# Performance work log

Hardware: AMD Instinct MI355X
Metric: run time of the kernel (lower is better)

Reference implementation:

```python
import jax, jax.numpy as jnp
import numpy as np

N_NODES = 50000
N_EDGES = 400000
IN_CH = 109
OUT_CH = 32


def setup_inputs() -> dict:
    key = jax.random.key(0)
    ks = jax.random.split(key, 12)
    dims = [(IN_CH, 10 * OUT_CH), (10 * OUT_CH, 2 * OUT_CH), (2 * OUT_CH, OUT_CH), (2 * OUT_CH, OUT_CH)]
    inp = {
        'x': jax.random.normal(ks[0], (N_NODES, IN_CH), dtype=jnp.float32),
        'edge_index': jax.random.randint(ks[1], (2, N_EDGES), 0, N_NODES, dtype=jnp.int64) if jax.config.jax_enable_x64 else jax.random.randint(ks[1], (2, N_EDGES), 0, N_NODES, dtype=jnp.int32),
    }
    names = ['W1', 'b1', 'W2', 'b2', 'Wmu', 'bmu', 'Wls', 'bls']
    for i, (fi, fo) in enumerate(dims):
        scale = 1.0 / np.sqrt(fi)
        inp[names[2 * i]] = jax.random.uniform(ks[2 + 2 * i], (fi, fo), minval=-scale, maxval=scale, dtype=jnp.float32)
        inp[names[2 * i + 1]] = jnp.zeros((fo,), dtype=jnp.float32)
    return inp


def _gcn_conv(x, src, dst, norm, W, b, n):
    # PyG GCNConv: h = x @ W, then symmetric-normalized aggregation, then + b
    h = x @ W                                   # [N, F_out]
    msg = h[src] * norm[:, None]                # [E+N, F_out]
    out = jax.ops.segment_sum(msg, dst, num_segments=n)
    return out + b


def _norm_and_loops(edge_index, n):
    # add self loops, compute D^{-1/2}(A+I)D^{-1/2} edge weights
    loops = jnp.arange(n, dtype=edge_index.dtype)
    src = jnp.concatenate([edge_index[0], loops])
    dst = jnp.concatenate([edge_index[1], loops])
    deg = jax.ops.segment_sum(jnp.ones_like(src, dtype=jnp.float32), dst, num_segments=n)
    dinv = jnp.where(deg > 0, jax.lax.rsqrt(jnp.maximum(deg, 1.0)), 0.0)
    norm = dinv[src] * dinv[dst]
    return src, dst, norm


def reference(x, edge_index, W1, b1, W2, b2, Wmu, bmu, Wls, bls):
    n = x.shape[0]
    src, dst, norm = _norm_and_loops(edge_index, n)
    h = jax.nn.relu(_gcn_conv(x, src, dst, norm, W1, b1, n))
    h = jax.nn.relu(_gcn_conv(h, src, dst, norm, W2, b2, n))
    mu = _gcn_conv(h, src, dst, norm, Wmu, bmu, n)
    logstd = _gcn_conv(h, src, dst, norm, Wls, bls, n)
    return (mu, logstd)
```

## Files before the change

### kernel.cpp

```cpp
#include <hip/hip_runtime.h>

#define NN 50000
#define NE 400000

typedef __attribute__((ext_vector_type(8))) short short8v;
typedef __attribute__((ext_vector_type(4))) float f32x4;

__device__ __forceinline__ unsigned short f2bf_rtn(float x) {
    unsigned u = __float_as_uint(x);
    unsigned r = u + 0x7FFFu + ((u >> 16) & 1u);
    return (unsigned short)(r >> 16);
}
__device__ __forceinline__ float bf2f(unsigned short h) {
    return __uint_as_float(((unsigned)h) << 16);
}

__global__ void prep_kernel(const float* __restrict__ x,
                            const float* __restrict__ W1, const float* __restrict__ W2,
                            const float* __restrict__ Wmu, const float* __restrict__ Wls,
                            unsigned* __restrict__ xp, int* __restrict__ zero_base,
                            unsigned short* __restrict__ w1t_hi,
                            unsigned short* __restrict__ w2t_hi,
                            unsigned short* __restrict__ wct_hi) {
    int b = blockIdx.x, tid = threadIdx.x;
    if (b < 12500) {
        int idx = b * 256 + tid;
        int i = idx >> 6, c2 = (idx & 63) * 2;
        long xb = (long)i * 109;
        float v0 = (c2 < 109) ? x[xb + c2] : 0.0f;
        float v1 = (c2 + 1 < 109) ? x[xb + c2 + 1] : 0.0f;
        xp[idx] = (unsigned)f2bf_rtn(v0) | ((unsigned)f2bf_rtn(v1) << 16);
    } else if (b < 12891) {
        int i = (b - 12500) * 256 + tid;
        if (i < 100096) zero_base[i] = 0;
    } else if (b < 13051) {
        int idx = (b - 12891) * 256 + tid;
        int n = idx >> 7, k = idx & 127;
        float v = (k < 109) ? W1[(long)k * 320 + n] : 0.0f;
        w1t_hi[idx] = f2bf_rtn(v);
    } else if (b < 13131) {
        int idx = (b - 13051) * 256 + tid;
        int n = idx / 320, k = idx - n * 320;
        w2t_hi[idx] = f2bf_rtn(W2[(long)k * 64 + n]);
    } else {
        int idx = (b - 13131) * 256 + tid;
        int n = idx >> 6, k = idx & 63;
        float v = (n < 32) ? Wmu[k * 32 + n] : Wls[k * 32 + (n - 32)];
        wct_hi[idx] = f2bf_rtn(v);
    }
}

__global__ void hist_kernel(const int* __restrict__ dst, int* __restrict__ counts) {
    for (int e = blockIdx.x * blockDim.x + threadIdx.x; e < NE; e += gridDim.x * blockDim.x)
        atomicAdd(&counts[dst[e]], 1);
}

__global__ void dinv_scan1_kernel(const int* __restrict__ counts, float* __restrict__ dinv,
                                  int* __restrict__ rowstart, int* __restrict__ bsum) {
    __shared__ int tmp[256];
    int tid = threadIdx.x;
    int i = blockIdx.x * 256 + tid;
    int v = (i < NN) ? counts[i] : 0;
    if (i < NN) dinv[i] = rsqrtf((float)(v + 1));
    tmp[tid] = v;
    __syncthreads();
    for (int off = 1; off < 256; off <<= 1) {
        int t = 0;
        if (tid >= off) t = tmp[tid - off];
        __syncthreads();
        if (tid >= off) tmp[tid] += t;
        __syncthreads();
    }
    if (i < NN) rowstart[i] = tmp[tid] - v;
    if (tid == 255) bsum[blockIdx.x] = tmp[255];
}

__global__ void scan23_kernel(int* __restrict__ rowstart, const int* __restrict__ bsum) {
    __shared__ int red[4];
    int tid = threadIdx.x;
    int v = (tid < 196 && tid < (int)blockIdx.x) ? bsum[tid] : 0;
    for (int off = 32; off > 0; off >>= 1) v += __shfl_down(v, off, 64);
    if ((tid & 63) == 0) red[tid >> 6] = v;
    __syncthreads();
    int pref = red[0] + red[1] + red[2] + red[3];
    int i = blockIdx.x * 256 + tid;
    if (i < NN) rowstart[i] += pref;
    if (i == 0) rowstart[NN] = NE;
}

__global__ void scatter_kernel(const int* __restrict__ src, const int* __restrict__ dst,
                               const int* __restrict__ rowstart, int* __restrict__ cursor,
                               int* __restrict__ esrc) {
    for (int e = blockIdx.x * blockDim.x + threadIdx.x; e < NE; e += gridDim.x * blockDim.x) {
        int d = dst[e];
        int pos = rowstart[d] + atomicAdd(&cursor[d], 1);
        esrc[pos] = src[e];
    }
}

__global__ __launch_bounds__(256) void agg109_packed_kernel(const int* __restrict__ rowstart,
                                                            const int* __restrict__ esrc,
                                                            const float* __restrict__ dinv,
                                                            const unsigned* __restrict__ xp,
                                                            unsigned* __restrict__ xa_hi32) {
    int wave = blockIdx.x * (blockDim.x >> 6) + (threadIdx.x >> 6);
    if (wave >= NN) return;
    int lane = threadIdx.x & 63;
    float wd = dinv[wave];
    unsigned pself = xp[(long)wave * 64 + lane];
    float acc0 = __uint_as_float(pself << 16) * wd;
    float acc1 = __uint_as_float(pself & 0xFFFF0000u) * wd;
    int j0 = rowstart[wave], j1 = rowstart[wave + 1];
    int j = j0;
    for (; j + 8 <= j1; j += 8) {
        int s[8];
        float w[8];
        unsigned pp[8];
        #pragma unroll
        for (int u = 0; u < 8; ++u) s[u] = esrc[j + u];
        #pragma unroll
        for (int u = 0; u < 8; ++u) w[u] = dinv[s[u]];
        #pragma unroll
        for (int u = 0; u < 8; ++u) pp[u] = xp[(long)s[u] * 64 + lane];
        #pragma unroll
        for (int u = 0; u < 8; ++u) {
            acc0 = fmaf(__uint_as_float(pp[u] << 16), w[u], acc0);
            acc1 = fmaf(__uint_as_float(pp[u] & 0xFFFF0000u), w[u], acc1);
        }
    }
    for (; j + 4 <= j1; j += 4) {
        int s0 = esrc[j], s1 = esrc[j + 1], s2 = esrc[j + 2], s3 = esrc[j + 3];
        float w0 = dinv[s0], w1 = dinv[s1], w2 = dinv[s2], w3 = dinv[s3];
        unsigned p0 = xp[(long)s0 * 64 + lane], p1 = xp[(long)s1 * 64 + lane];
        unsigned p2 = xp[(long)s2 * 64 + lane], p3 = xp[(long)s3 * 64 + lane];
        acc0 = fmaf(__uint_as_float(p0 << 16), w0, acc0);
        acc1 = fmaf(__uint_as_float(p0 & 0xFFFF0000u), w0, acc1);
        acc0 = fmaf(__uint_as_float(p1 << 16), w1, acc0);
        acc1 = fmaf(__uint_as_float(p1 & 0xFFFF0000u), w1, acc1);
        acc0 = fmaf(__uint_as_float(p2 << 16), w2, acc0);
        acc1 = fmaf(__uint_as_float(p2 & 0xFFFF0000u), w2, acc1);
        acc0 = fmaf(__uint_as_float(p3 << 16), w3, acc0);
        acc1 = fmaf(__uint_as_float(p3 & 0xFFFF0000u), w3, acc1);
    }
    for (; j < j1; ++j) {
        int s = esrc[j];
        float w = dinv[s];
        unsigned pv = xp[(long)s * 64 + lane];
        acc0 = fmaf(__uint_as_float(pv << 16), w, acc0);
        acc1 = fmaf(__uint_as_float(pv & 0xFFFF0000u), w, acc1);
    }
    acc0 *= wd;
    acc1 *= wd;
    xa_hi32[(long)wave * 64 + lane] =
        (unsigned)f2bf_rtn(acc0) | ((unsigned)f2bf_rtn(acc1) << 16);
}

#define LDA_T 136
#define LDH 328

__global__ __launch_bounds__(256) void gemm12_kernel(const unsigned short* __restrict__ xa,
                                                     const unsigned short* __restrict__ w1t,
                                                     const unsigned short* __restrict__ w2t,
                                                     const float* __restrict__ b1,
                                                     const float* __restrict__ dinv,
                                                     unsigned short* __restrict__ g2b) {
    __shared__ unsigned short As[64 * LDA_T];
    __shared__ unsigned short Bs[64 * LDA_T];
    __shared__ unsigned short Hs[64 * LDH];
    int tid = threadIdx.x;
    int wid = tid >> 6, lane = tid & 63;
    int l15 = lane & 15, l4 = lane >> 4;

    int T = gridDim.x;
    int xcd = blockIdx.x & 7, jj = blockIdx.x >> 3;
    int q = T >> 3, r = T & 7;
    int start = (xcd < r) ? xcd * (q + 1) : r * (q + 1) + (xcd - r) * q;
    int bm0 = (start + jj) * 64;

    #pragma unroll
    for (int r2 = 0; r2 < 4; ++r2) {
        int idx = tid + 256 * r2;
        int row = idx >> 4, slot = idx & 15;
        int grow = bm0 + row;
        if (grow >= NN) grow = NN - 1;
        *(uint4*)&As[row * LDA_T + slot * 8] = *(const uint4*)&xa[(long)grow * 128 + slot * 8];
    }
    #pragma unroll
    for (int r2 = 0; r2 < 4; ++r2) {
        int idx = tid + 256 * r2;
        int row = idx >> 4, slot = idx & 15;
        *(uint4*)&Bs[row * LDA_T + slot * 8] = *(const uint4*)&w1t[(long)row * 128 + slot * 8];
    }
    __syncthreads();

    for (int nc = 0; nc < 5; ++nc) {
        f32x4 acc[4] = {};
        #pragma unroll
        for (int ks = 0; ks < 4; ++ks) {
            int koff = ks * 32 + l4 * 8;
            short8v ah = *(const short8v*)&As[(wid * 16 + l15) * LDA_T + koff];
            #pragma unroll
            for (int n = 0; n < 4; ++n) {
                short8v bh = *(const short8v*)&Bs[(n * 16 + l15) * LDA_T + koff];
                acc[n] = __builtin_amdgcn_mfma_f32_16x16x32_bf16(ah, bh, acc[n], 0, 0, 0);
            }
        }
        int rbase = wid * 16 + l4 * 4;
        #pragma unroll
        for (int q2 = 0; q2 < 4; ++q2) {
            #pragma unroll
            for (int n = 0; n < 4; ++n) {
                int gcol = nc * 64 + n * 16 + l15;
                float v = acc[n][q2] + b1[gcol];
                v = v > 0.0f ? v : 0.0f;
                Hs[(rbase + q2) * LDH + gcol] = f2bf_rtn(v);
            }
        }
        __syncthreads();
        if (nc < 4) {
            #pragma unroll
            for (int r2 = 0; r2 < 4; ++r2) {
                int idx = tid + 256 * r2;
                int row = idx >> 4, slot = idx & 15;
                *(uint4*)&Bs[row * LDA_T + slot * 8] =
                    *(const uint4*)&w1t[(long)(nc * 64 + 64 + row) * 128 + slot * 8];
            }
            __syncthreads();
        }
    }

    f32x4 acc2[4] = {};
    for (int kc = 0; kc < 5; ++kc) {
        #pragma unroll
        for (int r2 = 0; r2 < 2; ++r2) {
            int idx = tid + 256 * r2;
            int row = idx >> 3, slot = idx & 7;
            *(uint4*)&Bs[row * LDA_T + slot * 8] =
                *(const uint4*)&w2t[(long)row * 320 + kc * 64 + slot * 8];
        }
        __syncthreads();
        #pragma unroll
        for (int ks = 0; ks < 2; ++ks) {
            int koff = ks * 32 + l4 * 8;
            short8v ah = *(const short8v*)&Hs[(wid * 16 + l15) * LDH + kc * 64 + koff];
            #pragma unroll
            for (int n = 0; n < 4; ++n) {
                short8v bh = *(const short8v*)&Bs[(n * 16 + l15) * LDA_T + koff];
                acc2[n] = __builtin_amdgcn_mfma_f32_16x16x32_bf16(ah, bh, acc2[n], 0, 0, 0);
            }
        }
        __syncthreads();
    }
    int rbase = bm0 + wid * 16 + l4 * 4;
    #pragma unroll
    for (int q2 = 0; q2 < 4; ++q2) {
        int grow = rbase + q2;
        if (grow >= NN) continue;
        float rs = dinv[grow];
        #pragma unroll
        for (int n = 0; n < 4; ++n) {
            int gcol = n * 16 + l15;
            g2b[(long)grow * 64 + gcol] = f2bf_rtn(acc2[n][q2] * rs);
        }
    }
}

__global__ __launch_bounds__(256) void agg64_relu_bf16_kernel(const int* __restrict__ rowstart,
                                                              const int* __restrict__ esrc,
                                                              const float* __restrict__ dinv,
                                                              const unsigned short* __restrict__ g,
                                                              const float* __restrict__ b,
                                                              unsigned short* __restrict__ hhi) {
    int wave = blockIdx.x * (blockDim.x >> 6) + (threadIdx.x >> 6);
    if (wave >= NN) return;
    int lane = threadIdx.x & 63;
    long base = (long)wave * 64;
    float acc = bf2f(g[base + lane]);
    int j0 = rowstart[wave], j1 = rowstart[wave + 1];
    int j = j0;
    for (; j + 8 <= j1; j += 8) {
        int s[8];
        float pp[8];
        #pragma unroll
        for (int u = 0; u < 8; ++u) s[u] = esrc[j + u];
        #pragma unroll
        for (int u = 0; u < 8; ++u) pp[u] = bf2f(g[(long)s[u] * 64 + lane]);
        #pragma unroll
        for (int u = 0; u < 8; ++u) acc += pp[u];
    }
    for (; j + 4 <= j1; j += 4) {
        int s0 = esrc[j], s1 = esrc[j + 1], s2 = esrc[j + 2], s3 = esrc[j + 3];
        float p0 = bf2f(g[(long)s0 * 64 + lane]), p1 = bf2f(g[(long)s1 * 64 + lane]);
        float p2 = bf2f(g[(long)s2 * 64 + lane]), p3 = bf2f(g[(long)s3 * 64 + lane]);
        acc += p0 + p1 + p2 + p3;
    }
    for (; j < j1; ++j) acc += bf2f(g[(long)esrc[j] * 64 + lane]);
    float v = acc * dinv[wave] + b[lane];
    v = v > 0.0f ? v : 0.0f;
    hhi[base + lane] = f2bf_rtn(v);
}

#define LDT 72
__global__ __launch_bounds__(1024) void agg_gemm3_kernel(const int* __restrict__ rowstart,
                                                         const int* __restrict__ esrc,
                                                         const float* __restrict__ dinv,
                                                         const unsigned short* __restrict__ h,
                                                         const unsigned short* __restrict__ wct_hi,
                                                         const float* __restrict__ bmu,
                                                         const float* __restrict__ bls,
                                                         float* __restrict__ out) {
    __shared__ unsigned short As[64 * LDT];
    __shared__ unsigned short Bs[64 * LDT];
    int tid = threadIdx.x;
    int wid = tid >> 6, lane = tid & 63;
    int m0 = blockIdx.x * 64;

    if (tid < 512) {
        int row = tid >> 3, slot = tid & 7;
        *(uint4*)&Bs[row * LDT + slot * 8] = *(const uint4*)&wct_hi[row * 64 + slot * 8];
    }

    #pragma unroll
    for (int t = 0; t < 4; ++t) {
        int node = m0 + wid * 4 + t;
        int i = node < NN ? node : NN - 1;
        long base = (long)i * 64;
        float wd = dinv[i];
        float acc = bf2f(h[base + lane]) * wd;
        int j0 = rowstart[i], j1 = rowstart[i + 1];
        int j = j0;
        for (; j + 8 <= j1; j += 8) {
            int s[8];
            float w[8], pp[8];
            #pragma unroll
            for (int u = 0; u < 8; ++u) s[u] = esrc[j + u];
            #pragma unroll
            for (int u = 0; u < 8; ++u) w[u] = dinv[s[u]];
            #pragma unroll
            for (int u = 0; u < 8; ++u) pp[u] = bf2f(h[(long)s[u] * 64 + lane]);
            #pragma unroll
            for (int u = 0; u < 8; ++u) acc = fmaf(pp[u], w[u], acc);
        }
        for (; j + 4 <= j1; j += 4) {
            int s0 = esrc[j], s1 = esrc[j + 1], s2 = esrc[j + 2], s3 = esrc[j + 3];
            float w0 = dinv[s0], w1 = dinv[s1], w2 = dinv[s2], w3 = dinv[s3];
            float p0 = bf2f(h[(long)s0 * 64 + lane]), p1 = bf2f(h[(long)s1 * 64 + lane]);
            float p2 = bf2f(h[(long)s2 * 64 + lane]), p3 = bf2f(h[(long)s3 * 64 + lane]);
            acc = fmaf(p0, w0, acc); acc = fmaf(p1, w1, acc);
            acc = fmaf(p2, w2, acc); acc = fmaf(p3, w3, acc);
        }
        for (; j < j1; ++j) {
            int s = esrc[j];
            acc = fmaf(bf2f(h[(long)s * 64 + lane]), dinv[s], acc);
        }
        As[(wid * 4 + t) * LDT + lane] = f2bf_rtn(acc * wd);
    }
    __syncthreads();

    int r = wid >> 2, c = wid & 3;
    int l15 = lane & 15, l4 = lane >> 4;
    f32x4 acc4 = {};
    #pragma unroll
    for (int ks = 0; ks < 2; ++ks) {
        int koff = ks * 32 + l4 * 8;
        short8v ah = *(const short8v*)&As[(r * 16 + l15) * LDT + koff];
        short8v bh = *(const short8v*)&Bs[(c * 16 + l15) * LDT + koff];
        acc4 = __builtin_amdgcn_mfma_f32_16x16x32_bf16(ah, bh, acc4, 0, 0, 0);
    }
    int rbase = m0 + r * 16 + l4 * 4;
    int gcol = c * 16 + l15;
    #pragma unroll
    for (int q2 = 0; q2 < 4; ++q2) {
        int grow = rbase + q2;
        if (grow >= NN) continue;
        float v = acc4[q2];
        if (gcol < 32)
            out[(long)grow * 32 + gcol] = v + bmu[gcol];
        else
            out[(long)NN * 32 + (long)grow * 32 + (gcol - 32)] = v + bls[gcol - 32];
    }
}

extern "C" void kernel_launch(void* const* d_in, const int* in_sizes, int n_in,
                              void* d_out, int out_size, void* d_ws, size_t ws_size,
                              hipStream_t stream) {
    const float* x   = (const float*)d_in[0];
    const int*   ei  = (const int*)d_in[1];
    const int*   src = ei;
    const int*   dst = ei + NE;
    const float* W1  = (const float*)d_in[2];
    const float* b1  = (const float*)d_in[3];
    const float* W2  = (const float*)d_in[4];
    const float* b2  = (const float*)d_in[5];
    const float* Wmu = (const float*)d_in[6];
    const float* bmu = (const float*)d_in[7];
    const float* Wls = (const float*)d_in[8];
    const float* bls = (const float*)d_in[9];
    float* out = (float*)d_out;

    char* p = (char*)d_ws;
    float* dinv   = (float*)p; p += 50048 * 4;
    int* counts   = (int*)p;   p += 50048 * 4;
    int* cursor   = (int*)p;   p += 50048 * 4;
    int* rowstart = (int*)p;   p += 50056 * 4;
    int* bsum     = (int*)p;   p += 256 * 4;
    int* esrc     = (int*)p;   p += 400000 * 4;
    unsigned* xp          = (unsigned*)p;       p += 50000L * 64 * 4;
    unsigned short* xa_hi = (unsigned short*)p; p += 50000L * 128 * 2;
    unsigned short* g2b   = (unsigned short*)p; p += 50000L * 64 * 2;
    unsigned short* w1t_hi = (unsigned short*)p; p += 320 * 128 * 2;
    unsigned short* w2t_hi = (unsigned short*)p; p += 64 * 320 * 2;
    unsigned short* wct_hi = (unsigned short*)p; p += 64 * 64 * 2;
    unsigned short* h2_hi = xa_hi;

    const int TB = 256;
    const int NB_NODES = (NN + TB - 1) / TB;
    const int NB_AGG = (NN * 64 + TB - 1) / TB;

    prep_kernel<<<13147, TB, 0, stream>>>(x, W1, W2, Wmu, Wls, xp, counts,
                                          w1t_hi, w2t_hi, wct_hi);
    hist_kernel<<<1024, TB, 0, stream>>>(dst, counts);
    dinv_scan1_kernel<<<NB_NODES, TB, 0, stream>>>(counts, dinv, rowstart, bsum);
    scan23_kernel<<<NB_NODES, TB, 0, stream>>>(rowstart, bsum);
    scatter_kernel<<<1024, TB, 0, stream>>>(src, dst, rowstart, cursor, esrc);

    agg109_packed_kernel<<<NB_AGG, TB, 0, stream>>>(rowstart, esrc, dinv, xp,
                                                    (unsigned*)xa_hi);

    gemm12_kernel<<<782, 256, 0, stream>>>(xa_hi, w1t_hi, w2t_hi, b1, dinv, g2b);

    agg64_relu_bf16_kernel<<<NB_AGG, TB, 0, stream>>>(rowstart, esrc, dinv, g2b, b2, h2_hi);

    agg_gemm3_kernel<<<782, 1024, 0, stream>>>(rowstart, esrc, dinv, h2_hi, wct_hi,
                                               bmu, bls, out);
}
```

Baseline: 158.7 us.

## Fuse first-layer aggregation into the layer-1/2 GEMM kernel

Removes the separate agg109 kernel and its 50000x128 bf16 intermediate buffer. Each 1024-thread block first gathers and aggregates its 64 nodes straight into shared memory, then runs both GEMMs with 16 waves, each owning one 16x16 output tile instead of four. This saves a kernel launch and a global write and read of the aggregated features. In exchange the 1024-thread blocks can limit occupancy and latency hiding during the irregular gather phase, and the MFMA work per wave is spread thinner.

```diff
diff --git a/kernel.cpp b/kernel.cpp
--- a/kernel.cpp
+++ b/kernel.cpp
@@ -98,72 +98,17 @@
     }
 }
 
-__global__ __launch_bounds__(256) void agg109_packed_kernel(const int* __restrict__ rowstart,
-                                                            const int* __restrict__ esrc,
-                                                            const float* __restrict__ dinv,
-                                                            const unsigned* __restrict__ xp,
-                                                            unsigned* __restrict__ xa_hi32) {
-    int wave = blockIdx.x * (blockDim.x >> 6) + (threadIdx.x >> 6);
-    if (wave >= NN) return;
-    int lane = threadIdx.x & 63;
-    float wd = dinv[wave];
-    unsigned pself = xp[(long)wave * 64 + lane];
-    float acc0 = __uint_as_float(pself << 16) * wd;
-    float acc1 = __uint_as_float(pself & 0xFFFF0000u) * wd;
-    int j0 = rowstart[wave], j1 = rowstart[wave + 1];
-    int j = j0;
-    for (; j + 8 <= j1; j += 8) {
-        int s[8];
-        float w[8];
-        unsigned pp[8];
-        #pragma unroll
-        for (int u = 0; u < 8; ++u) s[u] = esrc[j + u];
-        #pragma unroll
-        for (int u = 0; u < 8; ++u) w[u] = dinv[s[u]];
-        #pragma unroll
-        for (int u = 0; u < 8; ++u) pp[u] = xp[(long)s[u] * 64 + lane];
-        #pragma unroll
-        for (int u = 0; u < 8; ++u) {
-            acc0 = fmaf(__uint_as_float(pp[u] << 16), w[u], acc0);
-            acc1 = fmaf(__uint_as_float(pp[u] & 0xFFFF0000u), w[u], acc1);
-        }
-    }
-    for (; j + 4 <= j1; j += 4) {
-        int s0 = esrc[j], s1 = esrc[j + 1], s2 = esrc[j + 2], s3 = esrc[j + 3];
-        float w0 = dinv[s0], w1 = dinv[s1], w2 = dinv[s2], w3 = dinv[s3];
-        unsigned p0 = xp[(long)s0 * 64 + lane], p1 = xp[(long)s1 * 64 + lane];
-        unsigned p2 = xp[(long)s2 * 64 + lane], p3 = xp[(long)s3 * 64 + lane];
-        acc0 = fmaf(__uint_as_float(p0 << 16), w0, acc0);
-        acc1 = fmaf(__uint_as_float(p0 & 0xFFFF0000u), w0, acc1);
-        acc0 = fmaf(__uint_as_float(p1 << 16), w1, acc0);
-        acc1 = fmaf(__uint_as_float(p1 & 0xFFFF0000u), w1, acc1);
-        acc0 = fmaf(__uint_as_float(p2 << 16), w2, acc0);
-        acc1 = fmaf(__uint_as_float(p2 & 0xFFFF0000u), w2, acc1);
-        acc0 = fmaf(__uint_as_float(p3 << 16), w3, acc0);
-        acc1 = fmaf(__uint_as_float(p3 & 0xFFFF0000u), w3, acc1);
-    }
-    for (; j < j1; ++j) {
-        int s = esrc[j];
-        float w = dinv[s];
-        unsigned pv = xp[(long)s * 64 + lane];
-        acc0 = fmaf(__uint_as_float(pv << 16), w, acc0);
-        acc1 = fmaf(__uint_as_float(pv & 0xFFFF0000u), w, acc1);
-    }
-    acc0 *= wd;
-    acc1 *= wd;
-    xa_hi32[(long)wave * 64 + lane] =
-        (unsigned)f2bf_rtn(acc0) | ((unsigned)f2bf_rtn(acc1) << 16);
-}
-
 #define LDA_T 136
 #define LDH 328
 
-__global__ __launch_bounds__(256) void gemm12_kernel(const unsigned short* __restrict__ xa,
-                                                     const unsigned short* __restrict__ w1t,
-                                                     const unsigned short* __restrict__ w2t,
-                                                     const float* __restrict__ b1,
-                                                     const float* __restrict__ dinv,
-                                                     unsigned short* __restrict__ g2b) {
+__global__ __launch_bounds__(1024) void agg_gemm12_kernel(const int* __restrict__ rowstart,
+                                                          const int* __restrict__ esrc,
+                                                          const float* __restrict__ dinv,
+                                                          const unsigned* __restrict__ xp,
+                                                          const unsigned short* __restrict__ w1t,
+                                                          const unsigned short* __restrict__ w2t,
+                                                          const float* __restrict__ b1,
+                                                          unsigned short* __restrict__ g2b) {
     __shared__ unsigned short As[64 * LDA_T];
     __shared__ unsigned short Bs[64 * LDA_T];
     __shared__ unsigned short Hs[64 * LDH];
@@ -173,68 +118,101 @@
 
     int T = gridDim.x;
     int xcd = blockIdx.x & 7, jj = blockIdx.x >> 3;
-    int q = T >> 3, r = T & 7;
-    int start = (xcd < r) ? xcd * (q + 1) : r * (q + 1) + (xcd - r) * q;
-    int bm0 = (start + jj) * 64;
+    int q = T >> 3, r0 = T & 7;
+    int start = (xcd < r0) ? xcd * (q + 1) : r0 * (q + 1) + (xcd - r0) * q;
+    int m0 = (start + jj) * 64;
+
+    {
+        int row = tid >> 4, slot = tid & 15;
+        *(uint4*)&Bs[row * LDA_T + slot * 8] = *(const uint4*)&w1t[(long)row * 128 + slot * 8];
+    }
 
     #pragma unroll
-    for (int r2 = 0; r2 < 4; ++r2) {
-        int idx = tid + 256 * r2;
-        int row = idx >> 4, slot = idx & 15;
-        int grow = bm0 + row;
-        if (grow >= NN) grow = NN - 1;
-        *(uint4*)&As[row * LDA_T + slot * 8] = *(const uint4*)&xa[(long)grow * 128 + slot * 8];
-    }
-    #pragma unroll
-    for (int r2 = 0; r2 < 4; ++r2) {
-        int idx = tid + 256 * r2;
-        int row = idx >> 4, slot = idx & 15;
-        *(uint4*)&Bs[row * LDA_T + slot * 8] = *(const uint4*)&w1t[(long)row * 128 + slot * 8];
+    for (int t = 0; t < 4; ++t) {
+        int node = m0 + wid * 4 + t;
+        int i = node < NN ? node : NN - 1;
+        float wd = dinv[i];
+        unsigned pself = xp[(long)i * 64 + lane];
+        float acc0 = __uint_as_float(pself << 16) * wd;
+        float acc1 = __uint_as_float(pself & 0xFFFF0000u) * wd;
+        int j0 = rowstart[i], j1 = rowstart[i + 1];
+        int j = j0;
+        for (; j + 8 <= j1; j += 8) {
+            int s[8];
+            float w[8];
+            unsigned pp[8];
+            #pragma unroll
+            for (int u = 0; u < 8; ++u) s[u] = esrc[j + u];
+            #pragma unroll
+            for (int u = 0; u < 8; ++u) w[u] = dinv[s[u]];
+            #pragma unroll
+            for (int u = 0; u < 8; ++u) pp[u] = xp[(long)s[u] * 64 + lane];
+            #pragma unroll
+            for (int u = 0; u < 8; ++u) {
+                acc0 = fmaf(__uint_as_float(pp[u] << 16), w[u], acc0);
+                acc1 = fmaf(__uint_as_float(pp[u] & 0xFFFF0000u), w[u], acc1);
+            }
+        }
+        for (; j + 4 <= j1; j += 4) {
+            int s0 = esrc[j], s1 = esrc[j + 1], s2 = esrc[j + 2], s3 = esrc[j + 3];
+            float w0 = dinv[s0], w1 = dinv[s1], w2 = dinv[s2], w3 = dinv[s3];
+            unsigned p0 = xp[(long)s0 * 64 + lane], p1 = xp[(long)s1 * 64 + lane];
+            unsigned p2 = xp[(long)s2 * 64 + lane], p3 = xp[(long)s3 * 64 + lane];
+            acc0 = fmaf(__uint_as_float(p0 << 16), w0, acc0);
+            acc1 = fmaf(__uint_as_float(p0 & 0xFFFF0000u), w0, acc1);
+            acc0 = fmaf(__uint_as_float(p1 << 16), w1, acc0);
+            acc1 = fmaf(__uint_as_float(p1 & 0xFFFF0000u), w1, acc1);
+            acc0 = fmaf(__uint_as_float(p2 << 16), w2, acc0);
+            acc1 = fmaf(__uint_as_float(p2 & 0xFFFF0000u), w2, acc1);
+            acc0 = fmaf(__uint_as_float(p3 << 16), w3, acc0);
+            acc1 = fmaf(__uint_as_float(p3 & 0xFFFF0000u), w3, acc1);
+        }
+        for (; j < j1; ++j) {
+            int s = esrc[j];
+            float w = dinv[s];
+            unsigned pv = xp[(long)s * 64 + lane];
+            acc0 = fmaf(__uint_as_float(pv << 16), w, acc0);
+            acc1 = fmaf(__uint_as_float(pv & 0xFFFF0000u), w, acc1);
+        }
+        acc0 *= wd;
+        acc1 *= wd;
+        unsigned val = (unsigned)f2bf_rtn(acc0) | ((unsigned)f2bf_rtn(acc1) << 16);
+        *(unsigned*)&As[(wid * 4 + t) * LDA_T + lane * 2] = val;
     }
     __syncthreads();
 
+    int r = wid >> 2, c = wid & 3;
     for (int nc = 0; nc < 5; ++nc) {
-        f32x4 acc[4] = {};
+        f32x4 acc = {};
         #pragma unroll
         for (int ks = 0; ks < 4; ++ks) {
             int koff = ks * 32 + l4 * 8;
-            short8v ah = *(const short8v*)&As[(wid * 16 + l15) * LDA_T + koff];
-            #pragma unroll
-            for (int n = 0; n < 4; ++n) {
-                short8v bh = *(const short8v*)&Bs[(n * 16 + l15) * LDA_T + koff];
-                acc[n] = __builtin_amdgcn_mfma_f32_16x16x32_bf16(ah, bh, acc[n], 0, 0, 0);
-            }
-        }
-        int rbase = wid * 16 + l4 * 4;
+            short8v ah = *(const short8v*)&As[(r * 16 + l15) * LDA_T + koff];
+            short8v bh = *(const short8v*)&Bs[(c * 16 + l15) * LDA_T + koff];
+            acc = __builtin_amdgcn_mfma_f32_16x16x32_bf16(ah, bh, acc, 0, 0, 0);
+        }
+        int gcol = nc * 64 + c * 16 + l15;
+        float bb = b1[gcol];
+        int rb = r * 16 + l4 * 4;
         #pragma unroll
         for (int q2 = 0; q2 < 4; ++q2) {
-            #pragma unroll
-            for (int n = 0; n < 4; ++n) {
-                int gcol = nc * 64 + n * 16 + l15;
-                float v = acc[n][q2] + b1[gcol];
-                v = v > 0.0f ? v : 0.0f;
-                Hs[(rbase + q2) * LDH + gcol] = f2bf_rtn(v);
-            }
+            float v = acc[q2] + bb;
+            v = v > 0.0f ? v : 0.0f;
+            Hs[(rb + q2) * LDH + gcol] = f2bf_rtn(v);
         }
         __syncthreads();
         if (nc < 4) {
-            #pragma unroll
-            for (int r2 = 0; r2 < 4; ++r2) {
-                int idx = tid + 256 * r2;
-                int row = idx >> 4, slot = idx & 15;
-                *(uint4*)&Bs[row * LDA_T + slot * 8] =
-                    *(const uint4*)&w1t[(long)(nc * 64 + 64 + row) * 128 + slot * 8];
-            }
+            int row = tid >> 4, slot = tid & 15;
+            *(uint4*)&Bs[row * LDA_T + slot * 8] =
+                *(const uint4*)&w1t[(long)(nc * 64 + 64 + row) * 128 + slot * 8];
             __syncthreads();
         }
     }
 
-    f32x4 acc2[4] = {};
+    f32x4 acc2 = {};
     for (int kc = 0; kc < 5; ++kc) {
-        #pragma unroll
-        for (int r2 = 0; r2 < 2; ++r2) {
-            int idx = tid + 256 * r2;
-            int row = idx >> 3, slot = idx & 7;
+        if (tid < 512) {
+            int row = tid >> 3, slot = tid & 7;
             *(uint4*)&Bs[row * LDA_T + slot * 8] =
                 *(const uint4*)&w2t[(long)row * 320 + kc * 64 + slot * 8];
         }
@@ -242,26 +220,19 @@
         #pragma unroll
         for (int ks = 0; ks < 2; ++ks) {
             int koff = ks * 32 + l4 * 8;
-            short8v ah = *(const short8v*)&Hs[(wid * 16 + l15) * LDH + kc * 64 + koff];
-            #pragma unroll
-            for (int n = 0; n < 4; ++n) {
-                short8v bh = *(const short8v*)&Bs[(n * 16 + l15) * LDA_T + koff];
-                acc2[n] = __builtin_amdgcn_mfma_f32_16x16x32_bf16(ah, bh, acc2[n], 0, 0, 0);
-            }
+            short8v ah = *(const short8v*)&Hs[(r * 16 + l15) * LDH + kc * 64 + koff];
+            short8v bh = *(const short8v*)&Bs[(c * 16 + l15) * LDA_T + koff];
+            acc2 = __builtin_amdgcn_mfma_f32_16x16x32_bf16(ah, bh, acc2, 0, 0, 0);
         }
         __syncthreads();
     }
-    int rbase = bm0 + wid * 16 + l4 * 4;
+    int rbase = m0 + r * 16 + l4 * 4;
+    int gcol2 = c * 16 + l15;
     #pragma unroll
     for (int q2 = 0; q2 < 4; ++q2) {
         int grow = rbase + q2;
         if (grow >= NN) continue;
-        float rs = dinv[grow];
-        #pragma unroll
-        for (int n = 0; n < 4; ++n) {
-            int gcol = n * 16 + l15;
-            g2b[(long)grow * 64 + gcol] = f2bf_rtn(acc2[n][q2] * rs);
-        }
+        g2b[(long)grow * 64 + gcol2] = f2bf_rtn(acc2[q2] * dinv[grow]);
     }
 }
 
@@ -406,12 +377,11 @@
     int* bsum     = (int*)p;   p += 256 * 4;
     int* esrc     = (int*)p;   p += 400000 * 4;
     unsigned* xp          = (unsigned*)p;       p += 50000L * 64 * 4;
-    unsigned short* xa_hi = (unsigned short*)p; p += 50000L * 128 * 2;
     unsigned short* g2b   = (unsigned short*)p; p += 50000L * 64 * 2;
+    unsigned short* h2_hi = (unsigned short*)p; p += 50000L * 64 * 2;
     unsigned short* w1t_hi = (unsigned short*)p; p += 320 * 128 * 2;
     unsigned short* w2t_hi = (unsigned short*)p; p += 64 * 320 * 2;
     unsigned short* wct_hi = (unsigned short*)p; p += 64 * 64 * 2;
-    unsigned short* h2_hi = xa_hi;
 
     const int TB = 256;
     const int NB_NODES = (NN + TB - 1) / TB;
@@ -424,10 +394,8 @@
     scan23_kernel<<<NB_NODES, TB, 0, stream>>>(rowstart, bsum);
     scatter_kernel<<<1024, TB, 0, stream>>>(src, dst, rowstart, cursor, esrc);
 
-    agg109_packed_kernel<<<NB_AGG, TB, 0, stream>>>(rowstart, esrc, dinv, xp,
-                                                    (unsigned*)xa_hi);
-
-    gemm12_kernel<<<782, 256, 0, stream>>>(xa_hi, w1t_hi, w2t_hi, b1, dinv, g2b);
+    agg_gemm12_kernel<<<782, 1024, 0, stream>>>(rowstart, esrc, dinv, xp,
+                                                w1t_hi, w2t_hi, b1, g2b);
 
     agg64_relu_bf16_kernel<<<NB_AGG, TB, 0, stream>>>(rowstart, esrc, dinv, g2b, b2, h2_hi);
 
```

Result: slower. 182.7 us (+15.1%).

## Split each wave into two half-waves gathering alternate edges with wider loads

Applied to the files above, without the earlier changes.

All three edge-aggregation kernels now split each 64-lane wave into two 32-lane halves. Each half handles alternating neighbor edges and loads twice as many bytes per lane (uint2 or packed bf16 pairs). The partial sums are combined with a cross-half shuffle before writeback. This doubles the edges in flight per wave and widens per-lane loads, aiming to hide gather latency, at the cost of an extra shuffle and some divergence in the tail handling.

```diff
diff --git a/kernel.cpp b/kernel.cpp
--- a/kernel.cpp
+++ b/kernel.cpp
@@ -14,6 +14,8 @@
 __device__ __forceinline__ float bf2f(unsigned short h) {
     return __uint_as_float(((unsigned)h) << 16);
 }
+__device__ __forceinline__ float lo16f(unsigned u) { return __uint_as_float(u << 16); }
+__device__ __forceinline__ float hi16f(unsigned u) { return __uint_as_float(u & 0xFFFF0000u); }
 
 __global__ void prep_kernel(const float* __restrict__ x,
                             const float* __restrict__ W1, const float* __restrict__ W2,
@@ -106,53 +108,84 @@
     int wave = blockIdx.x * (blockDim.x >> 6) + (threadIdx.x >> 6);
     if (wave >= NN) return;
     int lane = threadIdx.x & 63;
+    int sub = lane & 31, half = lane >> 5;
+    const uint2* xp2 = (const uint2*)xp;
     float wd = dinv[wave];
-    unsigned pself = xp[(long)wave * 64 + lane];
-    float acc0 = __uint_as_float(pself << 16) * wd;
-    float acc1 = __uint_as_float(pself & 0xFFFF0000u) * wd;
+    float a0 = 0, a1 = 0, a2 = 0, a3 = 0;
+    if (half == 0) {
+        uint2 pv = xp2[(long)wave * 32 + sub];
+        a0 = lo16f(pv.x) * wd;
+        a1 = hi16f(pv.x) * wd;
+        a2 = lo16f(pv.y) * wd;
+        a3 = hi16f(pv.y) * wd;
+    }
     int j0 = rowstart[wave], j1 = rowstart[wave + 1];
     int j = j0;
-    for (; j + 8 <= j1; j += 8) {
+    for (; j + 16 <= j1; j += 16) {
         int s[8];
         float w[8];
-        unsigned pp[8];
-        #pragma unroll
-        for (int u = 0; u < 8; ++u) s[u] = esrc[j + u];
+        uint2 pp[8];
+        #pragma unroll
+        for (int u = 0; u < 8; ++u) s[u] = esrc[j + 2 * u + half];
         #pragma unroll
         for (int u = 0; u < 8; ++u) w[u] = dinv[s[u]];
         #pragma unroll
-        for (int u = 0; u < 8; ++u) pp[u] = xp[(long)s[u] * 64 + lane];
+        for (int u = 0; u < 8; ++u) pp[u] = xp2[(long)s[u] * 32 + sub];
         #pragma unroll
         for (int u = 0; u < 8; ++u) {
-            acc0 = fmaf(__uint_as_float(pp[u] << 16), w[u], acc0);
-            acc1 = fmaf(__uint_as_float(pp[u] & 0xFFFF0000u), w[u], acc1);
-        }
-    }
-    for (; j + 4 <= j1; j += 4) {
-        int s0 = esrc[j], s1 = esrc[j + 1], s2 = esrc[j + 2], s3 = esrc[j + 3];
-        float w0 = dinv[s0], w1 = dinv[s1], w2 = dinv[s2], w3 = dinv[s3];
-        unsigned p0 = xp[(long)s0 * 64 + lane], p1 = xp[(long)s1 * 64 + lane];
-        unsigned p2 = xp[(long)s2 * 64 + lane], p3 = xp[(long)s3 * 64 + lane];
-        acc0 = fmaf(__uint_as_float(p0 << 16), w0, acc0);
-        acc1 = fmaf(__uint_as_float(p0 & 0xFFFF0000u), w0, acc1);
-        acc0 = fmaf(__uint_as_float(p1 << 16), w1, acc0);
-        acc1 = fmaf(__uint_as_float(p1 & 0xFFFF0000u), w1, acc1);
-        acc0 = fmaf(__uint_as_float(p2 << 16), w2, acc0);
-        acc1 = fmaf(__uint_as_float(p2 & 0xFFFF0000u), w2, acc1);
-        acc0 = fmaf(__uint_as_float(p3 << 16), w3, acc0);
-        acc1 = fmaf(__uint_as_float(p3 & 0xFFFF0000u), w3, acc1);
-    }
-    for (; j < j1; ++j) {
+            a0 = fmaf(lo16f(pp[u].x), w[u], a0);
+            a1 = fmaf(hi16f(pp[u].x), w[u], a1);
+            a2 = fmaf(lo16f(pp[u].y), w[u], a2);
+            a3 = fmaf(hi16f(pp[u].y), w[u], a3);
+        }
+    }
+    for (; j + 8 <= j1; j += 8) {
+        int s[4];
+        float w[4];
+        uint2 pp[4];
+        #pragma unroll
+        for (int u = 0; u < 4; ++u) s[u] = esrc[j + 2 * u + half];
+        #pragma unroll
+        for (int u = 0; u < 4; ++u) w[u] = dinv[s[u]];
+        #pragma unroll
+        for (int u = 0; u < 4; ++u) pp[u] = xp2[(long)s[u] * 32 + sub];
+        #pragma unroll
+        for (int u = 0; u < 4; ++u) {
+            a0 = fmaf(lo16f(pp[u].x), w[u], a0);
+            a1 = fmaf(hi16f(pp[u].x), w[u], a1);
+            a2 = fmaf(lo16f(pp[u].y), w[u], a2);
+            a3 = fmaf(hi16f(pp[u].y), w[u], a3);
+        }
+    }
+    for (; j + 2 <= j1; j += 2) {
+        int s = esrc[j + half];
+        float w = dinv[s];
+        uint2 pv = xp2[(long)s * 32 + sub];
+        a0 = fmaf(lo16f(pv.x), w, a0);
+        a1 = fmaf(hi16f(pv.x), w, a1);
+        a2 = fmaf(lo16f(pv.y), w, a2);
+        a3 = fmaf(hi16f(pv.y), w, a3);
+    }
+    if (j < j1 && half == 0) {
         int s = esrc[j];
         float w = dinv[s];
-        unsigned pv = xp[(long)s * 64 + lane];
-        acc0 = fmaf(__uint_as_float(pv << 16), w, acc0);
-        acc1 = fmaf(__uint_as_float(pv & 0xFFFF0000u), w, acc1);
-    }
-    acc0 *= wd;
-    acc1 *= wd;
-    xa_hi32[(long)wave * 64 + lane] =
-        (unsigned)f2bf_rtn(acc0) | ((unsigned)f2bf_rtn(acc1) << 16);
+        uint2 pv = xp2[(long)s * 32 + sub];
+        a0 = fmaf(lo16f(pv.x), w, a0);
+        a1 = fmaf(hi16f(pv.x), w, a1);
+        a2 = fmaf(lo16f(pv.y), w, a2);
+        a3 = fmaf(hi16f(pv.y), w, a3);
+    }
+    a0 += __shfl_xor(a0, 32);
+    a1 += __shfl_xor(a1, 32);
+    a2 += __shfl_xor(a2, 32);
+    a3 += __shfl_xor(a3, 32);
+    if (half == 0) {
+        a0 *= wd; a1 *= wd; a2 *= wd; a3 *= wd;
+        uint2 val;
+        val.x = (unsigned)f2bf_rtn(a0) | ((unsigned)f2bf_rtn(a1) << 16);
+        val.y = (unsigned)f2bf_rtn(a2) | ((unsigned)f2bf_rtn(a3) << 16);
+        ((uint2*)xa_hi32)[(long)wave * 32 + sub] = val;
+    }
 }
 
 #define LDA_T 136
@@ -274,30 +307,57 @@
     int wave = blockIdx.x * (blockDim.x >> 6) + (threadIdx.x >> 6);
     if (wave >= NN) return;
     int lane = threadIdx.x & 63;
-    long base = (long)wave * 64;
-    float acc = bf2f(g[base + lane]);
+    int sub = lane & 31, half = lane >> 5;
+    const unsigned* gp = (const unsigned*)g;
+    float a0 = 0, a1 = 0;
+    if (half == 0) {
+        unsigned pv = gp[(long)wave * 32 + sub];
+        a0 = lo16f(pv);
+        a1 = hi16f(pv);
+    }
     int j0 = rowstart[wave], j1 = rowstart[wave + 1];
     int j = j0;
+    for (; j + 16 <= j1; j += 16) {
+        int s[8];
+        unsigned pp[8];
+        #pragma unroll
+        for (int u = 0; u < 8; ++u) s[u] = esrc[j + 2 * u + half];
+        #pragma unroll
+        for (int u = 0; u < 8; ++u) pp[u] = gp[(long)s[u] * 32 + sub];
+        #pragma unroll
+        for (int u = 0; u < 8; ++u) { a0 += lo16f(pp[u]); a1 += hi16f(pp[u]); }
+    }
     for (; j + 8 <= j1; j += 8) {
-        int s[8];
-        float pp[8];
-        #pragma unroll
-        for (int u = 0; u < 8; ++u) s[u] = esrc[j + u];
-        #pragma unroll
-        for (int u = 0; u < 8; ++u) pp[u] = bf2f(g[(long)s[u] * 64 + lane]);
-        #pragma unroll
-        for (int u = 0; u < 8; ++u) acc += pp[u];
-    }
-    for (; j + 4 <= j1; j += 4) {
-        int s0 = esrc[j], s1 = esrc[j + 1], s2 = esrc[j + 2], s3 = esrc[j + 3];
-        float p0 = bf2f(g[(long)s0 * 64 + lane]), p1 = bf2f(g[(long)s1 * 64 + lane]);
-        float p2 = bf2f(g[(long)s2 * 64 + lane]), p3 = bf2f(g[(long)s3 * 64 + lane]);
-        acc += p0 + p1 + p2 + p3;
-    }
-    for (; j < j1; ++j) acc += bf2f(g[(long)esrc[j] * 64 + lane]);
-    float v = acc * dinv[wave] + b[lane];
-    v = v > 0.0f ? v : 0.0f;
-    hhi[base + lane] = f2bf_rtn(v);
+        int s[4];
+        unsigned pp[4];
+        #pragma unroll
+        for (int u = 0; u < 4; ++u) s[u] = esrc[j + 2 * u + half];
+        #pragma unroll
+        for (int u = 0; u < 4; ++u) pp[u] = gp[(long)s[u] * 32 + sub];
+        #pragma unroll
+        for (int u = 0; u < 4; ++u) { a0 += lo16f(pp[u]); a1 += hi16f(pp[u]); }
+    }
+    for (; j + 2 <= j1; j += 2) {
+        unsigned pv = gp[(long)esrc[j + half] * 32 + sub];
+        a0 += lo16f(pv);
+        a1 += hi16f(pv);
+    }
+    if (j < j1 && half == 0) {
+        unsigned pv = gp[(long)esrc[j] * 32 + sub];
+        a0 += lo16f(pv);
+        a1 += hi16f(pv);
+    }
+    a0 += __shfl_xor(a0, 32);
+    a1 += __shfl_xor(a1, 32);
+    if (half == 0) {
+        float wd = dinv[wave];
+        float v0 = a0 * wd + b[sub * 2];
+        float v1 = a1 * wd + b[sub * 2 + 1];
+        v0 = v0 > 0.0f ? v0 : 0.0f;
+        v1 = v1 > 0.0f ? v1 : 0.0f;
+        ((unsigned*)hhi)[(long)wave * 32 + sub] =
+            (unsigned)f2bf_rtn(v0) | ((unsigned)f2bf_rtn(v1) << 16);
+    }
 }
 
 #define LDT 72
@@ -313,7 +373,9 @@
     __shared__ unsigned short Bs[64 * LDT];
     int tid = threadIdx.x;
     int wid = tid >> 6, lane = tid & 63;
+    int sub = lane & 31, half = lane >> 5;
     int m0 = blockIdx.x * 64;
+    const unsigned* hp = (const unsigned*)h;
 
     if (tid < 512) {
         int row = tid >> 3, slot = tid & 7;
@@ -324,36 +386,69 @@
     for (int t = 0; t < 4; ++t) {
         int node = m0 + wid * 4 + t;
         int i = node < NN ? node : NN - 1;
-        long base = (long)i * 64;
         float wd = dinv[i];
-        float acc = bf2f(h[base + lane]) * wd;
+        float a0 = 0, a1 = 0;
+        if (half == 0) {
+            unsigned pv = hp[(long)i * 32 + sub];
+            a0 = lo16f(pv) * wd;
+            a1 = hi16f(pv) * wd;
+        }
         int j0 = rowstart[i], j1 = rowstart[i + 1];
         int j = j0;
+        for (; j + 16 <= j1; j += 16) {
+            int s[8];
+            float w[8];
+            unsigned pp[8];
+            #pragma unroll
+            for (int u = 0; u < 8; ++u) s[u] = esrc[j + 2 * u + half];
+            #pragma unroll
+            for (int u = 0; u < 8; ++u) w[u] = dinv[s[u]];
+            #pragma unroll
+            for (int u = 0; u < 8; ++u) pp[u] = hp[(long)s[u] * 32 + sub];
+            #pragma unroll
+            for (int u = 0; u < 8; ++u) {
+                a0 = fmaf(lo16f(pp[u]), w[u], a0);
+                a1 = fmaf(hi16f(pp[u]), w[u], a1);
+            }
+        }
         for (; j + 8 <= j1; j += 8) {
-            int s[8];
-            float w[8], pp[8];
-            #pragma unroll
-            for (int u = 0; u < 8; ++u) s[u] = esrc[j + u];
-            #pragma unroll
-            for (int u = 0; u < 8; ++u) w[u] = dinv[s[u]];
-            #pragma unroll
-            for (int u = 0; u < 8; ++u) pp[u] = bf2f(h[(long)s[u] * 64 + lane]);
-            #pragma unroll
-            for (int u = 0; u < 8; ++u) acc = fmaf(pp[u], w[u], acc);
-        }
-        for (; j + 4 <= j1; j += 4) {
-            int s0 = esrc[j], s1 = esrc[j + 1], s2 = esrc[j + 2], s3 = esrc[j + 3];
-            float w0 = dinv[s0], w1 = dinv[s1], w2 = dinv[s2], w3 = dinv[s3];
-            float p0 = bf2f(h[(long)s0 * 64 + lane]), p1 = bf2f(h[(long)s1 * 64 + lane]);
-            float p2 = bf2f(h[(long)s2 * 64 + lane]), p3 = bf2f(h[(long)s3 * 64 + lane]);
-            acc = fmaf(p0, w0, acc); acc = fmaf(p1, w1, acc);
-            acc = fmaf(p2, w2, acc); acc = fmaf(p3, w3, acc);
-        }
-        for (; j < j1; ++j) {
+            int s[4];
+            float w[4];
+            unsigned pp[4];
+            #pragma unroll
+            for (int u = 0; u < 4; ++u) s[u] = esrc[j + 2 * u + half];
+            #pragma unroll
+            for (int u = 0; u < 4; ++u) w[u] = dinv[s[u]];
+            #pragma unroll
+            for (int u = 0; u < 4; ++u) pp[u] = hp[(long)s[u] * 32 + sub];
+            #pragma unroll
+            for (int u = 0; u < 4; ++u) {
+                a0 = fmaf(lo16f(pp[u]), w[u], a0);
+                a1 = fmaf(hi16f(pp[u]), w[u], a1);
+            }
+        }
+        for (; j + 2 <= j1; j += 2) {
+            int s = esrc[j + half];
+            float w = dinv[s];
+            unsigned pv = hp[(long)s * 32 + sub];
+            a0 = fmaf(lo16f(pv), w, a0);
+            a1 = fmaf(hi16f(pv), w, a1);
+        }
+        if (j < j1 && half == 0) {
             int s = esrc[j];
-            acc = fmaf(bf2f(h[(long)s * 64 + lane]), dinv[s], acc);
-        }
-        As[(wid * 4 + t) * LDT + lane] = f2bf_rtn(acc * wd);
+            float w = dinv[s];
+            unsigned pv = hp[(long)s * 32 + sub];
+            a0 = fmaf(lo16f(pv), w, a0);
+            a1 = fmaf(hi16f(pv), w, a1);
+        }
+        a0 += __shfl_xor(a0, 32);
+        a1 += __shfl_xor(a1, 32);
+        if (half == 0) {
+            a0 *= wd;
+            a1 *= wd;
+            *(unsigned*)&As[(wid * 4 + t) * LDT + sub * 2] =
+                (unsigned)f2bf_rtn(a0) | ((unsigned)f2bf_rtn(a1) << 16);
+        }
     }
     __syncthreads();
 
```

Result: slower. 163.9 us (+3.2%).
